# Kernel tuning notes

Measured on AMD Instinct MI355X. Metric: run time of the kernel, lower is better.

## Reference

```python
import jax, jax.numpy as jnp
import numpy as np
import math

B, L, DIN, DOUT = 4, 1024, 64, 10
D, N = 512, 16            # hidden_dim (d_model), state_dim (d_state)
R = math.ceil(D / 16)     # dt_rank = 32
DT_MIN, DT_MAX = 1e-3, 1e-1


def _mamba_params(key):
    k1, k2, k3 = jax.random.split(key, 3)
    xproj_w = jax.random.normal(k1, (R + 2 * N, D), jnp.float32) * (D ** -0.5)
    dt_std = R ** -0.5
    dtproj_w = jax.random.uniform(k2, (D, R), jnp.float32, -dt_std, dt_std)
    dt = jnp.exp(jax.random.uniform(k3, (D,), jnp.float32)
                 * (math.log(DT_MAX) - math.log(DT_MIN)) + math.log(DT_MIN))
    dt = jnp.clip(dt, 1e-4, None)
    dtproj_b = dt + jnp.log(-jnp.expm1(-dt))          # inverse softplus
    A_log = jnp.log(jnp.broadcast_to(jnp.arange(1, N + 1, dtype=jnp.float32), (D, N)))
    Dp = jnp.ones((D,), jnp.float32)
    return xproj_w, dtproj_w, dtproj_b, A_log, Dp


def setup_inputs() -> dict:
    key = jax.random.key(0)
    ks = jax.random.split(key, 8)
    inp = {
        'x': jax.random.normal(ks[0], (B, L, DIN), jnp.float32),
        'W_in': jax.random.normal(ks[1], (D, DIN), jnp.float32) * (DIN ** -0.5),
        'b_in': jnp.zeros((D,), jnp.float32),
        'mix1_w': jax.random.normal(ks[2], (D, D), jnp.float32) * (D ** -0.5),
        'mix1_b': jnp.zeros((D,), jnp.float32),
        'mix2_w': jax.random.normal(ks[3], (D, D), jnp.float32) * (D ** -0.5),
        'mix2_b': jnp.zeros((D,), jnp.float32),
        'out_w': jax.random.normal(ks[4], (DOUT, D), jnp.float32) * (D ** -0.5),
        'out_b': jnp.zeros((DOUT,), jnp.float32),
    }
    (inp['m1_xproj'], inp['m1_dtw'], inp['m1_dtb'], inp['m1_Alog'], inp['m1_D']) = _mamba_params(ks[5])
    (inp['m2_xproj'], inp['m2_dtw'], inp['m2_dtb'], inp['m2_Alog'], inp['m2_D']) = _mamba_params(ks[6])
    return inp


def mamba_block(h, xproj_w, dtproj_w, dtproj_b, A_log, Dp):
    # h: (b, l, d) ; selective scan with A = -exp(A_log), delta_softplus=True
    b, l, d = h.shape
    A = -jnp.exp(A_log)                              # (d, n)
    x_dbl = jnp.einsum('bld,rd->blr', h, xproj_w)    # (b, l, r+2n)
    dt, Bm, Cm = jnp.split(x_dbl, [R, R + N], axis=-1)
    delta = jax.nn.softplus(jnp.einsum('blr,dr->bld', dt, dtproj_w) + dtproj_b)  # (b,l,d)
    dA = jnp.exp(delta[..., None] * A)                               # (b,l,d,n)
    dBu = delta[..., None] * Bm[:, :, None, :] * h[..., None]        # (b,l,d,n)

    def step(hstate, inp_t):
        dA_t, dBu_t, C_t = inp_t                     # (b,d,n),(b,d,n),(b,n)
        hstate = dA_t * hstate + dBu_t
        y = jnp.einsum('bdn,bn->bd', hstate, C_t)
        return hstate, y

    h0 = jnp.zeros((b, d, N), h.dtype)
    _, ys = jax.lax.scan(step, h0,
                         (jnp.swapaxes(dA, 0, 1), jnp.swapaxes(dBu, 0, 1), jnp.swapaxes(Cm, 0, 1)))
    y = jnp.swapaxes(ys, 0, 1) + h * Dp              # (b, l, d)
    return y


def reference(x, W_in, b_in, m1_xproj, m1_dtw, m1_dtb, m1_Alog, m1_D,
              mix1_w, mix1_b, m2_xproj, m2_dtw, m2_dtb, m2_Alog, m2_D,
              mix2_w, mix2_b, out_w, out_b):
    h = jnp.einsum('bli,di->bld', x, W_in) + b_in
    y = h
    h = mamba_block(h, m1_xproj, m1_dtw, m1_dtb, m1_Alog, m1_D)
    h = jax.nn.gelu(h, approximate=False)
    h = jnp.einsum('bld,ed->ble', h, mix1_w) + mix1_b
    h = h + y
    y = h
    h = mamba_block(h, m2_xproj, m2_dtw, m2_dtb, m2_Alog, m2_D)
    h = jax.nn.gelu(h, approximate=False)
    h = jnp.einsum('bld,ed->ble', h, mix2_w) + mix2_b
    h = h + y
    h = h.mean(axis=1)                               # (b, d)
    return jnp.einsum('bd,od->bo', h, out_w) + out_b
```

## Files before the change

kernel.cpp:

```cpp
#include <hip/hip_runtime.h>
#include <math.h>

typedef unsigned short ushort_t;
typedef short bf8_t __attribute__((ext_vector_type(8)));
typedef float f4_t  __attribute__((ext_vector_type(4)));

constexpr int B_   = 4;
constexpr int L_   = 1024;
constexpr int DIN_ = 64;
constexpr int DOUT_= 10;
constexpr int D_   = 512;
constexpr int N_   = 16;
constexpr int R_   = 32;
constexpr int RN_  = 64;
constexpr int M_   = B_ * L_;

constexpr int CN_ = 64;
constexpr int CL_ = L_ / CN_;

__device__ float    g_h   [M_ * D_];
__device__ float    g_h2  [M_ * D_];
__device__ ushort_t g_hbf [M_ * D_];
__device__ ushort_t g_gelubf[M_ * D_];
__device__ float    g_xdbl[M_ * RN_];
__device__ float2   g_dc  [M_ * D_];
__device__ float    g_stL  [B_ * CN_ * D_ * N_];
__device__ float    g_sumd [B_ * CN_ * D_];
__device__ float    g_carry[B_ * CN_ * D_ * N_];
__device__ float    g_part [B_ * 16 * D_];
__device__ ushort_t g_w1bf [D_ * D_];
__device__ ushort_t g_w2bf [D_ * D_];
__device__ ushort_t g_xp1bf[RN_ * D_];
__device__ ushort_t g_xp2bf[RN_ * D_];

__device__ __forceinline__ float gelu_f(float x) {
  return 0.5f * x * (1.0f + erff(x * 0.7071067811865475f));
}
__device__ __forceinline__ float softplus_f(float x) {
  return fmaxf(x, 0.0f) + log1pf(__expf(-fabsf(x)));
}
__device__ __forceinline__ ushort_t f2bf(float x) {
  union { float f; unsigned u; } v; v.f = x;
  unsigned r = v.u + 0x7fffu + ((v.u >> 16) & 1u);
  return (ushort_t)(r >> 16);
}

__global__ __launch_bounds__(256) void k_cvt(const float* __restrict__ w1,
                                             const float* __restrict__ w2,
                                             const float* __restrict__ xp1,
                                             const float* __restrict__ xp2) {
  int i = (blockIdx.x * 256 + threadIdx.x) * 4;
  const float* src; ushort_t* dst; int off;
  if (i < 262144)      { src = w1;  dst = g_w1bf;  off = i; }
  else if (i < 524288) { src = w2;  dst = g_w2bf;  off = i - 262144; }
  else if (i < 557056) { src = xp1; dst = g_xp1bf; off = i - 524288; }
  else                 { src = xp2; dst = g_xp2bf; off = i - 557056; }
  float4 v = *(const float4*)&src[off];
  ushort4 o; o.x = f2bf(v.x); o.y = f2bf(v.y); o.z = f2bf(v.z); o.w = f2bf(v.w);
  *(ushort4*)&dst[off] = o;
}

template<int NN, int EPIM, bool DUAL>
__device__ __forceinline__ void gemm_bf16_dev(
    const ushort_t* __restrict__ Abf, const ushort_t* __restrict__ Wbf,
    const float* __restrict__ bias, const float* __restrict__ res,
    float* __restrict__ out, ushort_t* __restrict__ obf) {
  __shared__ ushort_t As[64][72];
  __shared__ ushort_t Bs[64][72];
  constexpr int NB = NN / 64;
  const int tid  = threadIdx.x;
  const int m0   = (blockIdx.x / NB) * 64;
  const int n0   = (blockIdx.x % NB) * 64;
  const int lane = tid & 63;
  const int wv   = tid >> 6;
  const int quad = lane >> 4;
  const int ln   = lane & 15;
  const int mw   = (wv & 1) * 32;
  const int nw   = (wv >> 1) * 32;

  f4_t acc[2][2] = {};

  for (int k0 = 0; k0 < 512; k0 += 64) {
#pragma unroll
    for (int c = 0; c < 2; ++c) {
      int idx = tid + c * 256;
      int m = idx >> 3, kq = (idx & 7) << 3;
      *(float4*)&As[m][kq] = *(const float4*)&Abf[(size_t)(m0 + m) * 512 + k0 + kq];
      *(float4*)&Bs[m][kq] = *(const float4*)&Wbf[(size_t)(n0 + m) * 512 + k0 + kq];
    }
    __syncthreads();
#pragma unroll
    for (int k1 = 0; k1 < 64; k1 += 32) {
      bf8_t a0 = *(const bf8_t*)&As[mw +      ln][k1 + quad * 8];
      bf8_t a1 = *(const bf8_t*)&As[mw + 16 + ln][k1 + quad * 8];
      bf8_t b0 = *(const bf8_t*)&Bs[nw +      ln][k1 + quad * 8];
      bf8_t b1 = *(const bf8_t*)&Bs[nw + 16 + ln][k1 + quad * 8];
      acc[0][0] = __builtin_amdgcn_mfma_f32_16x16x32_bf16(a0, b0, acc[0][0], 0, 0, 0);
      acc[0][1] = __builtin_amdgcn_mfma_f32_16x16x32_bf16(a0, b1, acc[0][1], 0, 0, 0);
      acc[1][0] = __builtin_amdgcn_mfma_f32_16x16x32_bf16(a1, b0, acc[1][0], 0, 0, 0);
      acc[1][1] = __builtin_amdgcn_mfma_f32_16x16x32_bf16(a1, b1, acc[1][1], 0, 0, 0);
    }
    __syncthreads();
  }

  float bj[2] = {0.f, 0.f};
  if constexpr (EPIM == 1) {
    bj[0] = bias[n0 + nw + ln];
    bj[1] = bias[n0 + nw + 16 + ln];
  }
#pragma unroll
  for (int i = 0; i < 2; ++i)
#pragma unroll
    for (int j = 0; j < 2; ++j) {
      const int nc = n0 + nw + 16 * j + ln;
#pragma unroll
      for (int r = 0; r < 4; ++r) {
        const int row = m0 + mw + 16 * i + quad * 4 + r;
        const size_t idx = (size_t)row * NN + nc;
        float v = acc[i][j][r];
        if constexpr (EPIM == 1) v += bj[j] + res[idx];
        out[idx] = v;
        if constexpr (DUAL) obf[idx] = f2bf(v);
      }
    }
}

__global__ __launch_bounds__(256) void k_xdbl1g() {
  gemm_bf16_dev<64, 0, false>(g_hbf, g_xp1bf, nullptr, nullptr, g_xdbl, nullptr);
}
__global__ __launch_bounds__(256) void k_xdbl2g() {
  gemm_bf16_dev<64, 0, false>(g_hbf, g_xp2bf, nullptr, nullptr, g_xdbl, nullptr);
}
__global__ __launch_bounds__(256) void k_mix1g(const float* __restrict__ bias) {
  gemm_bf16_dev<512, 1, true>(g_gelubf, g_w1bf, bias, g_h, g_h2, g_hbf);
}
__global__ __launch_bounds__(256) void k_mix2g(const float* __restrict__ bias) {
  gemm_bf16_dev<512, 1, false>(g_gelubf, g_w2bf, bias, g_h2, g_h, nullptr);
}

template<int K, int LDA, int NN, int EPI>
__device__ __forceinline__ void gemm_dev(const float* __restrict__ A,
                                         const float* __restrict__ Bt,
                                         const float* __restrict__ bias,
                                         const float* __restrict__ res,
                                         float* __restrict__ out,
                                         ushort_t* __restrict__ obf) {
  __shared__ float As[16][68];
  __shared__ float Bs[16][68];
  const int tid = threadIdx.x;
  const int tx = tid & 15;
  const int ty = tid >> 4;
  const int lm = tid >> 2;
  const int lk = (tid & 3) << 2;
  constexpr int NB = NN / 64;
  const int m0 = (blockIdx.x / NB) * 64;
  const int n0 = (blockIdx.x % NB) * 64;

  float acc[4][4] = {};
  for (int k0 = 0; k0 < K; k0 += 16) {
    float4 av = *(const float4*)&A[(size_t)(m0 + lm) * LDA + k0 + lk];
    float4 bv = *(const float4*)&Bt[(size_t)(n0 + lm) * K + k0 + lk];
    As[lk + 0][lm] = av.x; As[lk + 1][lm] = av.y;
    As[lk + 2][lm] = av.z; As[lk + 3][lm] = av.w;
    Bs[lk + 0][lm] = bv.x; Bs[lk + 1][lm] = bv.y;
    Bs[lk + 2][lm] = bv.z; Bs[lk + 3][lm] = bv.w;
    __syncthreads();
#pragma unroll
    for (int k = 0; k < 16; ++k) {
      float4 a = *(const float4*)&As[k][ty << 2];
      float4 b = *(const float4*)&Bs[k][tx << 2];
      float aa[4] = {a.x, a.y, a.z, a.w};
      float bb[4] = {b.x, b.y, b.z, b.w};
#pragma unroll
      for (int i = 0; i < 4; ++i)
#pragma unroll
        for (int j = 0; j < 4; ++j)
          acc[i][j] = fmaf(aa[i], bb[j], acc[i][j]);
    }
    __syncthreads();
  }

  const int nb = n0 + (tx << 2);
  float4 t = *(const float4*)&bias[nb];
  float b4[4] = {t.x, t.y, t.z, t.w};
#pragma unroll
  for (int i = 0; i < 4; ++i) {
    const int m = m0 + (ty << 2) + i;
    if constexpr (EPI == 2) {
      const float* hrow = &res[(size_t)m * NN];
      float2* o2 = (float2*)out;
#pragma unroll
      for (int j = 0; j < 4; ++j) {
        float delta = softplus_f(acc[i][j] + b4[j]);
        float c = delta * hrow[nb + j];
        o2[(size_t)m * NN + nb + j] = make_float2(delta, c);
      }
    } else {
      float4 v;
      v.x = acc[i][0] + b4[0];
      v.y = acc[i][1] + b4[1];
      v.z = acc[i][2] + b4[2];
      v.w = acc[i][3] + b4[3];
      *(float4*)&out[(size_t)m * NN + nb] = v;
      ushort4 o; o.x = f2bf(v.x); o.y = f2bf(v.y); o.z = f2bf(v.z); o.w = f2bf(v.w);
      *(ushort4*)&obf[(size_t)m * NN + nb] = o;
    }
  }
}

__device__ __forceinline__ void load_A(const float* __restrict__ Alog, int d,
                                       float* A) {
#pragma unroll
  for (int n = 0; n < 16; n += 4) {
    float4 t = *(const float4*)&Alog[d * N_ + n];
    A[n + 0] = -__expf(t.x); A[n + 1] = -__expf(t.y);
    A[n + 2] = -__expf(t.z); A[n + 3] = -__expf(t.w);
  }
}

__device__ __forceinline__ void scan_p1_dev(const float2* __restrict__ dc,
                                            const float*  __restrict__ xdbl,
                                            const float*  __restrict__ Alog) {
  __shared__ float sB[CL_][16];
  const int d = threadIdx.x;
  const int c = blockIdx.x & (CN_ - 1);
  const int b = blockIdx.x / CN_;
  const int row0 = b * L_ + c * CL_;
  if (threadIdx.x < CL_ * 16) {
    int l = threadIdx.x >> 4, n = threadIdx.x & 15;
    sB[l][n] = xdbl[(size_t)(row0 + l) * RN_ + R_ + n];
  }
  float A[16];
  load_A(Alog, d, A);
  __syncthreads();

  float st[16] = {};
  float sumd = 0.0f;
#pragma unroll
  for (int l = 0; l < CL_; ++l) {
    float2 dcv = dc[(size_t)(row0 + l) * D_ + d];
    sumd += dcv.x;
#pragma unroll
    for (int n = 0; n < 16; ++n) {
      float dA = __expf(dcv.x * A[n]);
      st[n] = fmaf(dA, st[n], dcv.y * sB[l][n]);
    }
  }
  const size_t o = ((size_t)(b * CN_ + c) * D_ + d) * N_;
#pragma unroll
  for (int n = 0; n < 16; n += 4)
    *(float4*)&g_stL[o + n] = make_float4(st[n], st[n+1], st[n+2], st[n+3]);
  g_sumd[(b * CN_ + c) * D_ + d] = sumd;
}

__global__ __launch_bounds__(256) void k_scan_carry(const float* __restrict__ Alog) {
  const int g = blockIdx.x * 256 + threadIdx.x;
  const int n = g & 15;
  const int d = (g >> 4) & (D_ - 1);
  const int b = g >> 13;
  const float A = -__expf(Alog[d * N_ + n]);
  float carry = 0.0f;
#pragma unroll 4
  for (int c = 0; c < CN_; ++c) {
    const size_t idx = ((size_t)(b * CN_ + c) * D_ + d) * N_ + n;
    g_carry[idx] = carry;
    float P = __expf(A * g_sumd[(b * CN_ + c) * D_ + d]);
    carry = fmaf(P, carry, g_stL[idx]);
  }
}

__device__ __forceinline__ void scan_p2_dev(const float2* __restrict__ dc,
                                            const float*  __restrict__ xdbl,
                                            const float*  __restrict__ h,
                                            const float*  __restrict__ Alog,
                                            const float*  __restrict__ Dp,
                                            ushort_t* __restrict__ ybf) {
  __shared__ float sBC[CL_][32];
  const int d = threadIdx.x;
  const int c = blockIdx.x & (CN_ - 1);
  const int b = blockIdx.x / CN_;
  const int row0 = b * L_ + c * CL_;
  {
    int l = threadIdx.x >> 5, idx = threadIdx.x & 31;
    sBC[l][idx] = xdbl[(size_t)(row0 + l) * RN_ + R_ + idx];
  }
  float A[16];
  load_A(Alog, d, A);
  const float Dpv = Dp[d];
  __syncthreads();

  float st[16];
  const size_t o = ((size_t)(b * CN_ + c) * D_ + d) * N_;
#pragma unroll
  for (int n = 0; n < 16; n += 4) {
    float4 t = *(const float4*)&g_carry[o + n];
    st[n] = t.x; st[n+1] = t.y; st[n+2] = t.z; st[n+3] = t.w;
  }
#pragma unroll
  for (int l = 0; l < CL_; ++l) {
    float2 dcv = dc[(size_t)(row0 + l) * D_ + d];
    float y = 0.0f;
#pragma unroll
    for (int n = 0; n < 16; ++n) {
      float dA = __expf(dcv.x * A[n]);
      st[n] = fmaf(dA, st[n], dcv.y * sBC[l][n]);
      y = fmaf(st[n], sBC[l][16 + n], y);
    }
    float hv = h[(size_t)(row0 + l) * D_ + d];
    ybf[(size_t)(row0 + l) * D_ + d] = f2bf(gelu_f(y + hv * Dpv));
  }
}

__global__ __launch_bounds__(256) void k_in(const float* x, const float* w, const float* b) {
  gemm_dev<64, 64, 512, 4>(x, w, b, nullptr, g_h, g_hbf);
}
__global__ __launch_bounds__(256) void k_delta1(const float* dtw, const float* dtb) {
  gemm_dev<32, 64, 512, 2>(g_xdbl, dtw, dtb, g_h, (float*)g_dc, nullptr);
}
__global__ __launch_bounds__(256) void k_delta2(const float* dtw, const float* dtb) {
  gemm_dev<32, 64, 512, 2>(g_xdbl, dtw, dtb, g_h2, (float*)g_dc, nullptr);
}
__global__ __launch_bounds__(512) void k_scan1_p1(const float* Alog) {
  scan_p1_dev(g_dc, g_xdbl, Alog);
}
__global__ __launch_bounds__(512) void k_scan1_p2(const float* Alog, const float* Dp) {
  scan_p2_dev(g_dc, g_xdbl, g_h, Alog, Dp, g_gelubf);
}
__global__ __launch_bounds__(512) void k_scan2_p1(const float* Alog) {
  scan_p1_dev(g_dc, g_xdbl, Alog);
}
__global__ __launch_bounds__(512) void k_scan2_p2(const float* Alog, const float* Dp) {
  scan_p2_dev(g_dc, g_xdbl, g_h2, Alog, Dp, g_gelubf);
}

__global__ __launch_bounds__(256) void k_finalA() {
  const int b = blockIdx.x >> 4, c = blockIdx.x & 15;
  const int row0 = b * L_ + c * 64;
  float s0 = 0.f, s1 = 0.f;
  for (int l = 0; l < 64; ++l) {
    s0 += g_h[(size_t)(row0 + l) * D_ + threadIdx.x];
    s1 += g_h[(size_t)(row0 + l) * D_ + threadIdx.x + 256];
  }
  g_part[(size_t)blockIdx.x * D_ + threadIdx.x] = s0;
  g_part[(size_t)blockIdx.x * D_ + threadIdx.x + 256] = s1;
}
__global__ __launch_bounds__(512) void k_finalB(const float* out_w, const float* out_b,
                                                float* out) {
  __shared__ float sm[D_];
  __shared__ float sp[DOUT_ * 16];
  const int b = blockIdx.x, tid = threadIdx.x;
  float s = 0.f;
#pragma unroll
  for (int c = 0; c < 16; ++c) s += g_part[(size_t)(b * 16 + c) * D_ + tid];
  sm[tid] = s * (1.0f / L_);
  __syncthreads();
  if (tid < DOUT_ * 16) {
    int o = tid >> 4, seg = tid & 15;
    float p = 0.0f;
#pragma unroll
    for (int i = 0; i < 32; ++i)
      p += sm[seg * 32 + i] * out_w[o * D_ + seg * 32 + i];
    sp[tid] = p;
  }
  __syncthreads();
  if (tid < DOUT_) {
    float v = out_b[tid];
#pragma unroll
    for (int i = 0; i < 16; ++i) v += sp[tid * 16 + i];
    out[b * DOUT_ + tid] = v;
  }
}

extern "C" void kernel_launch(void* const* d_in, const int* in_sizes, int n_in,
                              void* d_out, int out_size, void* d_ws, size_t ws_size,
                              hipStream_t stream) {
  const float* x        = (const float*)d_in[0];
  const float* W_in     = (const float*)d_in[1];
  const float* b_in     = (const float*)d_in[2];
  const float* mix1_w   = (const float*)d_in[3];
  const float* mix1_b   = (const float*)d_in[4];
  const float* mix2_w   = (const float*)d_in[5];
  const float* mix2_b   = (const float*)d_in[6];
  const float* out_w    = (const float*)d_in[7];
  const float* out_b    = (const float*)d_in[8];
  const float* m1_xproj = (const float*)d_in[9];
  const float* m1_dtw   = (const float*)d_in[10];
  const float* m1_dtb   = (const float*)d_in[11];
  const float* m1_Alog  = (const float*)d_in[12];
  const float* m1_D     = (const float*)d_in[13];
  const float* m2_xproj = (const float*)d_in[14];
  const float* m2_dtw   = (const float*)d_in[15];
  const float* m2_dtb   = (const float*)d_in[16];
  const float* m2_Alog  = (const float*)d_in[17];
  const float* m2_D     = (const float*)d_in[18];
  float* out = (float*)d_out;

  const int gFull  = (M_ / 64) * (D_ / 64);
  const int gScan  = B_ * CN_;
  const int gCarry = (B_ * D_ * N_) / 256;
  const int gMix   = (M_ / 64) * (D_ / 64);
  const int gXdbl  = (M_ / 64);

  k_cvt<<<576, 256, 0, stream>>>(mix1_w, mix2_w, m1_xproj, m2_xproj);
  k_in <<<gFull, 256, 0, stream>>>(x, W_in, b_in);

  k_xdbl1g  <<<gXdbl, 256, 0, stream>>>();
  k_delta1  <<<gFull, 256, 0, stream>>>(m1_dtw, m1_dtb);
  k_scan1_p1<<<gScan, 512, 0, stream>>>(m1_Alog);
  k_scan_carry<<<gCarry, 256, 0, stream>>>(m1_Alog);
  k_scan1_p2<<<gScan, 512, 0, stream>>>(m1_Alog, m1_D);
  k_mix1g   <<<gMix,  256, 0, stream>>>(mix1_b);
  k_xdbl2g  <<<gXdbl, 256, 0, stream>>>();
  k_delta2  <<<gFull, 256, 0, stream>>>(m2_dtw, m2_dtb);
  k_scan2_p1<<<gScan, 512, 0, stream>>>(m2_Alog);
  k_scan_carry<<<gCarry, 256, 0, stream>>>(m2_Alog);
  k_scan2_p2<<<gScan, 512, 0, stream>>>(m2_Alog, m2_D);
  k_mix2g   <<<gMix,  256, 0, stream>>>(mix2_b);
  k_finalA<<<B_ * 16, 256, 0, stream>>>();
  k_finalB<<<B_,      512, 0, stream>>>(out_w, out_b, out);
}
```

Before: 250.0 us.

## Fuse delta projection into scan pass one, MFMA input GEMM, fold mean into mix2

Computes the dt projection and softplus inside the first scan pass per chunk, so the separate delta GEMM kernel goes away along with its launches. The pass still writes g_dc for the second pass. The input projection now runs as a bf16 MFMA kernel instead of the fp32 SIMT GEMM, which adds bf16 rounding of x and W_in. The sequence mean is accumulated with atomics in the mix2 GEMM epilogue, removing the finalA pass over g_h. g_mean is zeroed by an extra block in the convert kernel.

```diff
diff --git a/kernel.cpp b/kernel.cpp
--- a/kernel.cpp
+++ b/kernel.cpp
@@ -27,7 +27,7 @@
 __device__ float    g_stL  [B_ * CN_ * D_ * N_];
 __device__ float    g_sumd [B_ * CN_ * D_];
 __device__ float    g_carry[B_ * CN_ * D_ * N_];
-__device__ float    g_part [B_ * 16 * D_];
+__device__ float    g_mean [B_ * D_];
 __device__ ushort_t g_w1bf [D_ * D_];
 __device__ ushort_t g_w2bf [D_ * D_];
 __device__ ushort_t g_xp1bf[RN_ * D_];
@@ -49,6 +49,11 @@
                                              const float* __restrict__ w2,
                                              const float* __restrict__ xp1,
                                              const float* __restrict__ xp2) {
+  if (blockIdx.x == 576) {
+#pragma unroll
+    for (int j = 0; j < 8; ++j) g_mean[threadIdx.x * 8 + j] = 0.0f;
+    return;
+  }
   int i = (blockIdx.x * 256 + threadIdx.x) * 4;
   const float* src; ushort_t* dst; int off;
   if (i < 262144)      { src = w1;  dst = g_w1bf;  off = i; }
@@ -60,7 +65,7 @@
   *(ushort4*)&dst[off] = o;
 }
 
-template<int NN, int EPIM, bool DUAL>
+template<int NN, int EPIM, bool DUAL, bool MEAN>
 __device__ __forceinline__ void gemm_bf16_dev(
     const ushort_t* __restrict__ Abf, const ushort_t* __restrict__ Wbf,
     const float* __restrict__ bias, const float* __restrict__ res,
@@ -108,6 +113,7 @@
     bj[0] = bias[n0 + nw + ln];
     bj[1] = bias[n0 + nw + 16 + ln];
   }
+  float psum[2][2] = {{0.f, 0.f}, {0.f, 0.f}};
 #pragma unroll
   for (int i = 0; i < 2; ++i)
 #pragma unroll
@@ -121,91 +127,101 @@
         if constexpr (EPIM == 1) v += bj[j] + res[idx];
         out[idx] = v;
         if constexpr (DUAL) obf[idx] = f2bf(v);
+        if constexpr (MEAN) psum[i][j] += v;
       }
     }
+  if constexpr (MEAN) {
+    __shared__ float ssum[16][64];
+#pragma unroll
+    for (int i = 0; i < 2; ++i)
+#pragma unroll
+      for (int j = 0; j < 2; ++j) {
+        const int rg = (wv & 1) * 8 + i * 4 + quad;
+        const int cl = (wv >> 1) * 32 + j * 16 + ln;
+        ssum[rg][cl] = psum[i][j];
+      }
+    __syncthreads();
+    if (tid < 64) {
+      float s = 0.f;
+#pragma unroll
+      for (int rg = 0; rg < 16; ++rg) s += ssum[rg][tid];
+      const int b = m0 >> 10;
+      atomicAdd(&g_mean[b * D_ + n0 + tid], s);
+    }
+  }
 }
 
 __global__ __launch_bounds__(256) void k_xdbl1g() {
-  gemm_bf16_dev<64, 0, false>(g_hbf, g_xp1bf, nullptr, nullptr, g_xdbl, nullptr);
+  gemm_bf16_dev<64, 0, false, false>(g_hbf, g_xp1bf, nullptr, nullptr, g_xdbl, nullptr);
 }
 __global__ __launch_bounds__(256) void k_xdbl2g() {
-  gemm_bf16_dev<64, 0, false>(g_hbf, g_xp2bf, nullptr, nullptr, g_xdbl, nullptr);
+  gemm_bf16_dev<64, 0, false, false>(g_hbf, g_xp2bf, nullptr, nullptr, g_xdbl, nullptr);
 }
 __global__ __launch_bounds__(256) void k_mix1g(const float* __restrict__ bias) {
-  gemm_bf16_dev<512, 1, true>(g_gelubf, g_w1bf, bias, g_h, g_h2, g_hbf);
+  gemm_bf16_dev<512, 1, true, false>(g_gelubf, g_w1bf, bias, g_h, g_h2, g_hbf);
 }
 __global__ __launch_bounds__(256) void k_mix2g(const float* __restrict__ bias) {
-  gemm_bf16_dev<512, 1, false>(g_gelubf, g_w2bf, bias, g_h2, g_h, nullptr);
-}
-
-template<int K, int LDA, int NN, int EPI>
-__device__ __forceinline__ void gemm_dev(const float* __restrict__ A,
-                                         const float* __restrict__ Bt,
-                                         const float* __restrict__ bias,
-                                         const float* __restrict__ res,
-                                         float* __restrict__ out,
-                                         ushort_t* __restrict__ obf) {
-  __shared__ float As[16][68];
-  __shared__ float Bs[16][68];
-  const int tid = threadIdx.x;
-  const int tx = tid & 15;
-  const int ty = tid >> 4;
-  const int lm = tid >> 2;
-  const int lk = (tid & 3) << 2;
-  constexpr int NB = NN / 64;
-  const int m0 = (blockIdx.x / NB) * 64;
-  const int n0 = (blockIdx.x % NB) * 64;
-
-  float acc[4][4] = {};
-  for (int k0 = 0; k0 < K; k0 += 16) {
-    float4 av = *(const float4*)&A[(size_t)(m0 + lm) * LDA + k0 + lk];
-    float4 bv = *(const float4*)&Bt[(size_t)(n0 + lm) * K + k0 + lk];
-    As[lk + 0][lm] = av.x; As[lk + 1][lm] = av.y;
-    As[lk + 2][lm] = av.z; As[lk + 3][lm] = av.w;
-    Bs[lk + 0][lm] = bv.x; Bs[lk + 1][lm] = bv.y;
-    Bs[lk + 2][lm] = bv.z; Bs[lk + 3][lm] = bv.w;
-    __syncthreads();
-#pragma unroll
-    for (int k = 0; k < 16; ++k) {
-      float4 a = *(const float4*)&As[k][ty << 2];
-      float4 b = *(const float4*)&Bs[k][tx << 2];
-      float aa[4] = {a.x, a.y, a.z, a.w};
-      float bb[4] = {b.x, b.y, b.z, b.w};
-#pragma unroll
-      for (int i = 0; i < 4; ++i)
-#pragma unroll
-        for (int j = 0; j < 4; ++j)
-          acc[i][j] = fmaf(aa[i], bb[j], acc[i][j]);
-    }
-    __syncthreads();
-  }
-
-  const int nb = n0 + (tx << 2);
-  float4 t = *(const float4*)&bias[nb];
-  float b4[4] = {t.x, t.y, t.z, t.w};
-#pragma unroll
-  for (int i = 0; i < 4; ++i) {
-    const int m = m0 + (ty << 2) + i;
-    if constexpr (EPI == 2) {
-      const float* hrow = &res[(size_t)m * NN];
-      float2* o2 = (float2*)out;
-#pragma unroll
-      for (int j = 0; j < 4; ++j) {
-        float delta = softplus_f(acc[i][j] + b4[j]);
-        float c = delta * hrow[nb + j];
-        o2[(size_t)m * NN + nb + j] = make_float2(delta, c);
+  gemm_bf16_dev<512, 1, false, true>(g_gelubf, g_w2bf, bias, g_h2, g_h, nullptr);
+}
+
+__global__ __launch_bounds__(256) void k_in_mfma(const float* __restrict__ x,
+                                                 const float* __restrict__ w,
+                                                 const float* __restrict__ bias) {
+  __shared__ ushort_t As[64][72];
+  __shared__ ushort_t Bs[64][72];
+  const int tid  = threadIdx.x;
+  const int m0   = (blockIdx.x >> 3) * 64;
+  const int n0   = (blockIdx.x & 7) * 64;
+  const int lane = tid & 63;
+  const int wv   = tid >> 6;
+  const int quad = lane >> 4;
+  const int ln   = lane & 15;
+  const int mw   = (wv & 1) * 32;
+  const int nw   = (wv >> 1) * 32;
+
+  {
+    const int m = tid >> 2, q = (tid & 3) << 4;
+#pragma unroll
+    for (int i = 0; i < 4; ++i) {
+      float4 va = *(const float4*)&x[(size_t)(m0 + m) * 64 + q + i * 4];
+      float4 vb = *(const float4*)&w[(size_t)(n0 + m) * 64 + q + i * 4];
+      ushort4 oa, ob;
+      oa.x = f2bf(va.x); oa.y = f2bf(va.y); oa.z = f2bf(va.z); oa.w = f2bf(va.w);
+      ob.x = f2bf(vb.x); ob.y = f2bf(vb.y); ob.z = f2bf(vb.z); ob.w = f2bf(vb.w);
+      *(ushort4*)&As[m][q + i * 4] = oa;
+      *(ushort4*)&Bs[m][q + i * 4] = ob;
+    }
+  }
+  __syncthreads();
+
+  f4_t acc[2][2] = {};
+#pragma unroll
+  for (int k1 = 0; k1 < 64; k1 += 32) {
+    bf8_t a0 = *(const bf8_t*)&As[mw +      ln][k1 + quad * 8];
+    bf8_t a1 = *(const bf8_t*)&As[mw + 16 + ln][k1 + quad * 8];
+    bf8_t b0 = *(const bf8_t*)&Bs[nw +      ln][k1 + quad * 8];
+    bf8_t b1 = *(const bf8_t*)&Bs[nw + 16 + ln][k1 + quad * 8];
+    acc[0][0] = __builtin_amdgcn_mfma_f32_16x16x32_bf16(a0, b0, acc[0][0], 0, 0, 0);
+    acc[0][1] = __builtin_amdgcn_mfma_f32_16x16x32_bf16(a0, b1, acc[0][1], 0, 0, 0);
+    acc[1][0] = __builtin_amdgcn_mfma_f32_16x16x32_bf16(a1, b0, acc[1][0], 0, 0, 0);
+    acc[1][1] = __builtin_amdgcn_mfma_f32_16x16x32_bf16(a1, b1, acc[1][1], 0, 0, 0);
+  }
+
+  float bj[2] = { bias[n0 + nw + ln], bias[n0 + nw + 16 + ln] };
+#pragma unroll
+  for (int i = 0; i < 2; ++i)
+#pragma unroll
+    for (int j = 0; j < 2; ++j) {
+      const int nc = n0 + nw + 16 * j + ln;
+#pragma unroll
+      for (int r = 0; r < 4; ++r) {
+        const int row = m0 + mw + 16 * i + quad * 4 + r;
+        const size_t idx = (size_t)row * D_ + nc;
+        float v = acc[i][j][r] + bj[j];
+        g_h[idx] = v;
+        g_hbf[idx] = f2bf(v);
       }
-    } else {
-      float4 v;
-      v.x = acc[i][0] + b4[0];
-      v.y = acc[i][1] + b4[1];
-      v.z = acc[i][2] + b4[2];
-      v.w = acc[i][3] + b4[3];
-      *(float4*)&out[(size_t)m * NN + nb] = v;
-      ushort4 o; o.x = f2bf(v.x); o.y = f2bf(v.y); o.z = f2bf(v.z); o.w = f2bf(v.w);
-      *(ushort4*)&obf[(size_t)m * NN + nb] = o;
-    }
-  }
+    }
 }
 
 __device__ __forceinline__ void load_A(const float* __restrict__ Alog, int d,
@@ -218,18 +234,29 @@
   }
 }
 
-__device__ __forceinline__ void scan_p1_dev(const float2* __restrict__ dc,
-                                            const float*  __restrict__ xdbl,
-                                            const float*  __restrict__ Alog) {
-  __shared__ float sB[CL_][16];
+__device__ __forceinline__ void dscan_p1_dev(const float* __restrict__ h,
+                                             const float* __restrict__ dtw,
+                                             const float* __restrict__ dtb,
+                                             const float* __restrict__ Alog) {
+  __shared__ float sdt[CL_][33];
+  __shared__ float sB [CL_][16];
   const int d = threadIdx.x;
   const int c = blockIdx.x & (CN_ - 1);
   const int b = blockIdx.x / CN_;
   const int row0 = b * L_ + c * CL_;
-  if (threadIdx.x < CL_ * 16) {
-    int l = threadIdx.x >> 4, n = threadIdx.x & 15;
-    sB[l][n] = xdbl[(size_t)(row0 + l) * RN_ + R_ + n];
-  }
+
+  { int l = d >> 5, k = d & 31; sdt[l][k] = g_xdbl[(size_t)(row0 + l) * RN_ + k]; }
+  if (d < CL_ * 16) {
+    int l = d >> 4, n = d & 15;
+    sB[l][n] = g_xdbl[(size_t)(row0 + l) * RN_ + R_ + n];
+  }
+  float w[32];
+#pragma unroll
+  for (int r = 0; r < 32; r += 4) {
+    float4 t = *(const float4*)&dtw[d * R_ + r];
+    w[r] = t.x; w[r + 1] = t.y; w[r + 2] = t.z; w[r + 3] = t.w;
+  }
+  const float bias = dtb[d];
   float A[16];
   load_A(Alog, d, A);
   __syncthreads();
@@ -238,12 +265,18 @@
   float sumd = 0.0f;
 #pragma unroll
   for (int l = 0; l < CL_; ++l) {
-    float2 dcv = dc[(size_t)(row0 + l) * D_ + d];
-    sumd += dcv.x;
+    float acc = bias;
+#pragma unroll
+    for (int k = 0; k < 32; ++k) acc = fmaf(sdt[l][k], w[k], acc);
+    const float delta = softplus_f(acc);
+    const float hv = h[(size_t)(row0 + l) * D_ + d];
+    const float dh = delta * hv;
+    g_dc[(size_t)(row0 + l) * D_ + d] = make_float2(delta, dh);
+    sumd += delta;
 #pragma unroll
     for (int n = 0; n < 16; ++n) {
-      float dA = __expf(dcv.x * A[n]);
-      st[n] = fmaf(dA, st[n], dcv.y * sB[l][n]);
+      float dA = __expf(delta * A[n]);
+      st[n] = fmaf(dA, st[n], dh * sB[l][n]);
     }
   }
   const size_t o = ((size_t)(b * CN_ + c) * D_ + d) * N_;
@@ -251,6 +284,15 @@
   for (int n = 0; n < 16; n += 4)
     *(float4*)&g_stL[o + n] = make_float4(st[n], st[n+1], st[n+2], st[n+3]);
   g_sumd[(b * CN_ + c) * D_ + d] = sumd;
+}
+
+__global__ __launch_bounds__(512) void k_dscan1(const float* dtw, const float* dtb,
+                                                const float* Alog) {
+  dscan_p1_dev(g_h, dtw, dtb, Alog);
+}
+__global__ __launch_bounds__(512) void k_dscan2(const float* dtw, const float* dtb,
+                                                const float* Alog) {
+  dscan_p1_dev(g_h2, dtw, dtb, Alog);
 }
 
 __global__ __launch_bounds__(256) void k_scan_carry(const float* __restrict__ Alog) {
@@ -311,48 +353,19 @@
   }
 }
 
-__global__ __launch_bounds__(256) void k_in(const float* x, const float* w, const float* b) {
-  gemm_dev<64, 64, 512, 4>(x, w, b, nullptr, g_h, g_hbf);
-}
-__global__ __launch_bounds__(256) void k_delta1(const float* dtw, const float* dtb) {
-  gemm_dev<32, 64, 512, 2>(g_xdbl, dtw, dtb, g_h, (float*)g_dc, nullptr);
-}
-__global__ __launch_bounds__(256) void k_delta2(const float* dtw, const float* dtb) {
-  gemm_dev<32, 64, 512, 2>(g_xdbl, dtw, dtb, g_h2, (float*)g_dc, nullptr);
-}
-__global__ __launch_bounds__(512) void k_scan1_p1(const float* Alog) {
-  scan_p1_dev(g_dc, g_xdbl, Alog);
-}
 __global__ __launch_bounds__(512) void k_scan1_p2(const float* Alog, const float* Dp) {
   scan_p2_dev(g_dc, g_xdbl, g_h, Alog, Dp, g_gelubf);
 }
-__global__ __launch_bounds__(512) void k_scan2_p1(const float* Alog) {
-  scan_p1_dev(g_dc, g_xdbl, Alog);
-}
 __global__ __launch_bounds__(512) void k_scan2_p2(const float* Alog, const float* Dp) {
   scan_p2_dev(g_dc, g_xdbl, g_h2, Alog, Dp, g_gelubf);
 }
 
-__global__ __launch_bounds__(256) void k_finalA() {
-  const int b = blockIdx.x >> 4, c = blockIdx.x & 15;
-  const int row0 = b * L_ + c * 64;
-  float s0 = 0.f, s1 = 0.f;
-  for (int l = 0; l < 64; ++l) {
-    s0 += g_h[(size_t)(row0 + l) * D_ + threadIdx.x];
-    s1 += g_h[(size_t)(row0 + l) * D_ + threadIdx.x + 256];
-  }
-  g_part[(size_t)blockIdx.x * D_ + threadIdx.x] = s0;
-  g_part[(size_t)blockIdx.x * D_ + threadIdx.x + 256] = s1;
-}
 __global__ __launch_bounds__(512) void k_finalB(const float* out_w, const float* out_b,
                                                 float* out) {
   __shared__ float sm[D_];
   __shared__ float sp[DOUT_ * 16];
   const int b = blockIdx.x, tid = threadIdx.x;
-  float s = 0.f;
-#pragma unroll
-  for (int c = 0; c < 16; ++c) s += g_part[(size_t)(b * 16 + c) * D_ + tid];
-  sm[tid] = s * (1.0f / L_);
+  sm[tid] = g_mean[b * D_ + tid] * (1.0f / L_);
   __syncthreads();
   if (tid < DOUT_ * 16) {
     int o = tid >> 4, seg = tid & 15;
@@ -395,27 +408,23 @@
   const float* m2_D     = (const float*)d_in[18];
   float* out = (float*)d_out;
 
-  const int gFull  = (M_ / 64) * (D_ / 64);
   const int gScan  = B_ * CN_;
   const int gCarry = (B_ * D_ * N_) / 256;
   const int gMix   = (M_ / 64) * (D_ / 64);
   const int gXdbl  = (M_ / 64);
 
-  k_cvt<<<576, 256, 0, stream>>>(mix1_w, mix2_w, m1_xproj, m2_xproj);
-  k_in <<<gFull, 256, 0, stream>>>(x, W_in, b_in);
+  k_cvt    <<<577,  256, 0, stream>>>(mix1_w, mix2_w, m1_xproj, m2_xproj);
+  k_in_mfma<<<gMix, 256, 0, stream>>>(x, W_in, b_in);
 
   k_xdbl1g  <<<gXdbl, 256, 0, stream>>>();
-  k_delta1  <<<gFull, 256, 0, stream>>>(m1_dtw, m1_dtb);
-  k_scan1_p1<<<gScan, 512, 0, stream>>>(m1_Alog);
+  k_dscan1  <<<gScan, 512, 0, stream>>>(m1_dtw, m1_dtb, m1_Alog);
   k_scan_carry<<<gCarry, 256, 0, stream>>>(m1_Alog);
   k_scan1_p2<<<gScan, 512, 0, stream>>>(m1_Alog, m1_D);
   k_mix1g   <<<gMix,  256, 0, stream>>>(mix1_b);
   k_xdbl2g  <<<gXdbl, 256, 0, stream>>>();
-  k_delta2  <<<gFull, 256, 0, stream>>>(m2_dtw, m2_dtb);
-  k_scan2_p1<<<gScan, 512, 0, stream>>>(m2_Alog);
+  k_dscan2  <<<gScan, 512, 0, stream>>>(m2_dtw, m2_dtb, m2_Alog);
   k_scan_carry<<<gCarry, 256, 0, stream>>>(m2_Alog);
   k_scan2_p2<<<gScan, 512, 0, stream>>>(m2_Alog, m2_D);
   k_mix2g   <<<gMix,  256, 0, stream>>>(mix2_b);
-  k_finalA<<<B_ * 16, 256, 0, stream>>>();
-  k_finalB<<<B_,      512, 0, stream>>>(out_w, out_b, out);
-}
+  k_finalB<<<B_, 512, 0, stream>>>(out_w, out_b, out);
+}
```

Result: faster. 244.6 us (-2.2%).
